# Kernel optimization log

Measured on AMD Instinct MI355X. Metric: run time of the kernel, lower is better.

Reference implementation:

```python
import jax, jax.numpy as jnp
import numpy as np

B, T, D = 2, 2048, 2048
H, KVH, HD = 32, 8, 64
N_REP = H // KVH


def setup_inputs() -> dict:
    key = jax.random.key(0)
    ks = jax.random.split(key, 7)
    x = jax.random.normal(ks[0], (B, T, D), dtype=jnp.float32)
    # rope tables: [max_seq, head_dim//2]
    cos = jax.random.uniform(ks[1], (T, HD // 2), dtype=jnp.float32, minval=-1.0, maxval=1.0)
    sin = jax.random.uniform(ks[2], (T, HD // 2), dtype=jnp.float32, minval=-1.0, maxval=1.0)
    s = 0.02
    wq = jax.random.normal(ks[3], (D, H * HD), dtype=jnp.float32) * s
    wk = jax.random.normal(ks[4], (D, KVH * HD), dtype=jnp.float32) * s
    wv = jax.random.normal(ks[5], (D, KVH * HD), dtype=jnp.float32) * s
    wo = jax.random.normal(ks[6], (H * HD, D), dtype=jnp.float32) * s
    return {"x": x, "cos": cos, "sin": sin, "wq": wq, "wk": wk, "wv": wv, "wo": wo}


def _rotate(t):
    h = t.shape[-1] // 2
    return jnp.concatenate([-t[..., h:], t[..., :h]], axis=-1)


def reference(x, cos, sin, wq, wk, wv, wo):
    b, t, _ = x.shape
    # projections -> [B, heads, T, HD]
    q = (x @ wq).reshape(b, t, H, HD).transpose(0, 2, 1, 3)
    k = (x @ wk).reshape(b, t, KVH, HD).transpose(0, 2, 1, 3)
    v = (x @ wv).reshape(b, t, KVH, HD).transpose(0, 2, 1, 3)
    # rope: cos/sin tiled (concat) to full head_dim, broadcast over batch/head
    cos_f = jnp.tile(cos[:t], (1, 2))[None, None]  # [1,1,T,HD]
    sin_f = jnp.tile(sin[:t], (1, 2))[None, None]
    q = q * cos_f + _rotate(q) * sin_f
    k = k * cos_f + _rotate(k) * sin_f
    # GQA: repeat kv heads
    k = jnp.repeat(k, N_REP, axis=1)
    v = jnp.repeat(v, N_REP, axis=1)
    scale = 1.0 / np.sqrt(HD).astype(np.float32)
    scores = jnp.einsum('bhqd,bhkd->bhqk', q, k) * scale
    causal = jnp.tril(jnp.ones((t, t), dtype=bool))
    scores = jnp.where(causal, scores, jnp.float32(-1e30))
    attn = jax.nn.softmax(scores, axis=-1)
    out = jnp.einsum('bhqk,bhkd->bhqd', attn, v)
    out = out.transpose(0, 2, 1, 3).reshape(b, t, H * HD)
    return out @ wo
```

## Files before the change

### kernel.cpp

```cpp
#include <hip/hip_runtime.h>
#include <hip/hip_bf16.h>
#include <cstdint>

typedef unsigned short u16;
typedef unsigned int u32;
typedef __bf16 bf16x8 __attribute__((ext_vector_type(8)));
typedef float f32x4 __attribute__((ext_vector_type(4)));
typedef float f32x16 __attribute__((ext_vector_type(16)));

#define BATCH 2
#define SEQ 2048
#define DMODEL 2048
#define NH 32
#define NKVH 8
#define HD 64
#define NQROWS (BATCH*SEQ)
#define QCOLS (NH*HD)
#define KVCOLS (NKVH*HD)
#define NCAT (QCOLS+2*KVCOLS)

static __device__ __forceinline__ u16 f2bf(float f) {
  u32 u = __float_as_uint(f);
  return (u16)((u + 0x7fffu + ((u >> 16) & 1u)) >> 16);
}
static __device__ __forceinline__ float bf2f(u16 h) {
  return __uint_as_float(((u32)h) << 16);
}

#define GLOAD16(gp, lp) __builtin_amdgcn_global_load_lds( \
    (const __attribute__((address_space(1))) void*)(gp),  \
    (__attribute__((address_space(3))) void*)(lp), 16, 0, 0)

__global__ __launch_bounds__(256) void k_cvt_bf16(const float* __restrict__ in,
                                                  u16* __restrict__ out, int n4) {
  int i = blockIdx.x * 256 + threadIdx.x;
  if (i >= n4) return;
  float4 v = reinterpret_cast<const float4*>(in)[i];
  ushort4 o;
  o.x = f2bf(v.x); o.y = f2bf(v.y); o.z = f2bf(v.z); o.w = f2bf(v.w);
  reinterpret_cast<ushort4*>(out)[i] = o;
}

__global__ __launch_bounds__(256) void k_transpose_w(const float* __restrict__ in,
                                                     u16* __restrict__ out, int R, int C) {
  __shared__ float tile[32][33];
  int c0 = blockIdx.x * 32, r0 = blockIdx.y * 32;
  int tx = threadIdx.x, ty = threadIdx.y;
#pragma unroll
  for (int i = 0; i < 4; i++)
    tile[ty * 4 + i][tx] = in[(size_t)(r0 + ty * 4 + i) * C + c0 + tx];
  __syncthreads();
#pragma unroll
  for (int i = 0; i < 4; i++)
    out[(size_t)(c0 + ty * 4 + i) * R + r0 + tx] = f2bf(tile[tx][ty * 4 + i]);
}

template<int EPI>
__global__ __launch_bounds__(256) void k_gemm(const u16* __restrict__ A,
                                              const u16* __restrict__ BT,
                                              void* __restrict__ Cout,
                                              int M, int N, int K,
                                              const float* __restrict__ cosb,
                                              const float* __restrict__ sinb,
                                              u16* __restrict__ dstK,
                                              u16* __restrict__ dstV) {
  __shared__ __align__(16) u16 As[128 * 32];
  __shared__ __align__(16) u16 Bs[128 * 32];
  const int tid = threadIdx.x;
  const int w = tid >> 6, l = tid & 63;
  const int l15 = l & 15, l4 = l >> 4;
  const int m0 = blockIdx.y * 128, n0 = blockIdx.x * 128;
  const int wr = w >> 1, wc = w & 1;

  const u16* ga = A + (size_t)(m0 + w * 32 + (l >> 2)) * K + (l & 3) * 8;
  const u16* gb = BT + (size_t)(n0 + w * 32 + (l >> 2)) * K + (l & 3) * 8;
  u16* asb = &As[w * 1024];
  u16* bsb = &Bs[w * 1024];
  const int af_off = (wr * 64 + l15) * 32 + l4 * 8;
  const int bf_off = (wc * 64 + l15) * 32 + l4 * 8;

  f32x4 acc[4][4] = {};
  for (int kt = 0; kt < K; kt += 32) {
    GLOAD16(ga, asb);
    GLOAD16(ga + 16 * (size_t)K, asb + 512);
    GLOAD16(gb, bsb);
    GLOAD16(gb + 16 * (size_t)K, bsb + 512);
    ga += 32; gb += 32;
    __syncthreads();
    bf16x8 af[4], bfv[4];
#pragma unroll
    for (int mi = 0; mi < 4; mi++)
      af[mi] = *reinterpret_cast<const bf16x8*>(&As[af_off + mi * 512]);
#pragma unroll
    for (int ni = 0; ni < 4; ni++)
      bfv[ni] = *reinterpret_cast<const bf16x8*>(&Bs[bf_off + ni * 512]);
#pragma unroll
    for (int mi = 0; mi < 4; mi++)
#pragma unroll
      for (int ni = 0; ni < 4; ni++)
        acc[mi][ni] = __builtin_amdgcn_mfma_f32_16x16x32_bf16(af[mi], bfv[ni], acc[mi][ni], 0, 0, 0);
    __syncthreads();
  }

  const int row0 = m0 + wr * 64 + l4 * 4;
  const int col0 = n0 + wc * 64 + l15;
  if constexpr (EPI == 1) {
    float* C = (float*)Cout;
#pragma unroll
    for (int mi = 0; mi < 4; mi++)
#pragma unroll
      for (int ni = 0; ni < 4; ni++)
#pragma unroll
        for (int j = 0; j < 4; j++)
          C[(size_t)(row0 + mi * 16 + j) * N + col0 + ni * 16] = acc[mi][ni][j];
  } else {
    if (n0 < QCOLS + KVCOLS) {
#pragma unroll
      for (int mi = 0; mi < 4; mi++)
#pragma unroll
        for (int j = 0; j < 4; j++) {
          int t = (row0 + mi * 16 + j) & (SEQ - 1);
#pragma unroll
          for (int ni = 0; ni < 2; ni++) {
            int d = ni * 16 + l15;
            float c = cosb[t * 32 + d], s = sinb[t * 32 + d];
            float a = acc[mi][ni][j], bb = acc[mi][ni + 2][j];
            acc[mi][ni][j]     = a * c - bb * s;
            acc[mi][ni + 2][j] = bb * c + a * s;
          }
        }
      if (n0 < QCOLS) {
        u16* C = (u16*)Cout;
#pragma unroll
        for (int mi = 0; mi < 4; mi++)
#pragma unroll
          for (int ni = 0; ni < 4; ni++)
#pragma unroll
            for (int j = 0; j < 4; j++)
              C[(size_t)(row0 + mi * 16 + j) * QCOLS + col0 + ni * 16] = f2bf(acc[mi][ni][j]);
      } else {
        int kc0 = col0 - QCOLS;
#pragma unroll
        for (int mi = 0; mi < 4; mi++)
#pragma unroll
          for (int ni = 0; ni < 4; ni++)
#pragma unroll
            for (int j = 0; j < 4; j++)
              dstK[(size_t)(row0 + mi * 16 + j) * KVCOLS + kc0 + ni * 16] = f2bf(acc[mi][ni][j]);
      }
    } else {
      int vc0 = col0 - (QCOLS + KVCOLS);
#pragma unroll
      for (int mi = 0; mi < 4; mi++) {
        int row = row0 + mi * 16;
        int b = row >> 11, t = row & (SEQ - 1);
#pragma unroll
        for (int ni = 0; ni < 4; ni++) {
          ushort4 v;
          v.x = f2bf(acc[mi][ni][0]);
          v.y = f2bf(acc[mi][ni][1]);
          v.z = f2bf(acc[mi][ni][2]);
          v.w = f2bf(acc[mi][ni][3]);
          *reinterpret_cast<ushort4*>(&dstV[((size_t)b * KVCOLS + vc0 + ni * 16) * SEQ + t]) = v;
        }
      }
    }
  }
}

__global__ __launch_bounds__(128, 3) void k_attn(const u16* __restrict__ Q,
                                                 const u16* __restrict__ K,
                                                 const u16* __restrict__ VT,
                                                 u16* __restrict__ AO) {
  __shared__ __align__(16) u16 Ks[2][4096];
  __shared__ __align__(16) u16 Vs[2][4096];
  const int tid = threadIdx.x;
  const int w = tid >> 6, l = tid & 63;
  const int lo = l & 31, hi = l >> 5;
  const int bh = blockIdx.y;
  const int b = bh >> 5, h = bh & 31, g = h >> 2;
  const float cS2 = 0.125f * 1.44269504088896f;
  const int srow = l >> 3;
  const int scol = l & 7;

  const u16* Kbase = K + ((size_t)b * SEQ) * KVCOLS + g * 64;
  const u16* Vbase = VT + ((size_t)(b * KVCOLS + g * 64)) * SEQ;

  for (int half = 0; half < 2; half++) {
    const int qt = half ? (31 - blockIdx.x) : blockIdx.x;
    const int qbase = qt * 64 + w * 32;
    const int nkc = qt + 1;
    const int qloc = w * 32 + lo;

    bf16x8 qf[4];
    {
      const u16* qp = Q + (size_t)(b * SEQ + qbase + lo) * QCOLS + h * 64 + hi * 8;
#pragma unroll
      for (int kb = 0; kb < 4; kb++) {
        union { bf16x8 v; u16 s[8]; } in_, out_;
        in_.v = *reinterpret_cast<const bf16x8*>(qp + kb * 16);
#pragma unroll
        for (int e = 0; e < 8; e++) out_.s[e] = f2bf(bf2f(in_.s[e]) * cS2);
        qf[kb] = out_.v;
      }
    }
    f32x16 oacc[2] = {};
    float ls0 = 0.f, ls1 = 0.f;

#pragma unroll
    for (int i = 0; i < 4; i++) {
      int r = w * 32 + i * 8 + srow;
      int cs = scol ^ (srow & 7);
      GLOAD16(Kbase + (size_t)r * KVCOLS + cs * 8, &Ks[0][(w * 32 + i * 8) * 64 + l * 8]);
      GLOAD16(Vbase + (size_t)r * SEQ + cs * 8, &Vs[0][(w * 32 + i * 8) * 64 + l * 8]);
    }
    __syncthreads();

    for (int kc = 0; kc < nkc; kc++) {
      const int bi = kc & 1;
      if (kc + 1 < nkc) {
#pragma unroll
        for (int i = 0; i < 4; i++) {
          int r = w * 32 + i * 8 + srow;
          int cs = scol ^ (srow & 7);
          GLOAD16(Kbase + (size_t)((kc + 1) * 64 + r) * KVCOLS + cs * 8,
                  &Ks[bi ^ 1][(w * 32 + i * 8) * 64 + l * 8]);
          GLOAD16(Vbase + (size_t)r * SEQ + (kc + 1) * 64 + cs * 8,
                  &Vs[bi ^ 1][(w * 32 + i * 8) * 64 + l * 8]);
        }
      }
      f32x16 sacc[2] = {};
      __builtin_amdgcn_s_setprio(1);
#pragma unroll
      for (int t = 0; t < 2; t++) {
#pragma unroll
        for (int kb = 0; kb < 4; kb++) {
          int row = t * 32 + lo;
          int slot = (2 * kb + hi) ^ (lo & 7);
          bf16x8 kf = *reinterpret_cast<const bf16x8*>(&Ks[bi][row * 64 + slot * 8]);
          sacc[t] = __builtin_amdgcn_mfma_f32_32x32x16_bf16(kf, qf[kb], sacc[t], 0, 0, 0);
        }
      }
      __builtin_amdgcn_s_setprio(0);

      const bool diag = (kc == qt);
      u32 u[2][4][2];
#pragma unroll
      for (int t = 0; t < 2; t++) {
        float pv[16];
#pragma unroll
        for (int r = 0; r < 16; r++) {
          float e = exp2f(sacc[t][r]);
          if (diag) {
            int kvoff = t * 32 + (r & 3) + 8 * (r >> 2) + 4 * hi;
            if (kvoff > qloc) e = 0.f;
          }
          pv[r] = e;
          if (t == 0) ls0 += e; else ls1 += e;
        }
#pragma unroll
        for (int qd = 0; qd < 4; qd++)
#pragma unroll
          for (int hh = 0; hh < 2; hh++) {
            u32 uu;
            asm("v_cvt_pk_bf16_f32 %0, %1, %2"
                : "=v"(uu) : "v"(pv[qd * 4 + 2 * hh]), "v"(pv[qd * 4 + 2 * hh + 1]));
            u[t][qd][hh] = uu;
          }
      }

#pragma unroll
      for (int km = 0; km < 4; km++) {
        const int t = km >> 1, p = km & 1;
        u32 a0 = u[t][2 * p][0], b0 = u[t][2 * p + 1][0];
        u32 a1 = u[t][2 * p][1], b1 = u[t][2 * p + 1][1];
        asm("v_permlane32_swap_b32 %0, %1" : "+v"(a0), "+v"(b0));
        asm("v_permlane32_swap_b32 %0, %1" : "+v"(a1), "+v"(b1));
        union { u32 uu[4]; bf16x8 v; } pa;
        pa.uu[0] = a0; pa.uu[1] = a1; pa.uu[2] = b0; pa.uu[3] = b1;
        __builtin_amdgcn_s_setprio(1);
#pragma unroll
        for (int td = 0; td < 2; td++) {
          int row = td * 32 + lo;
          int slot = (2 * km + hi) ^ (lo & 7);
          bf16x8 vf = *reinterpret_cast<const bf16x8*>(&Vs[bi][row * 64 + slot * 8]);
          oacc[td] = __builtin_amdgcn_mfma_f32_32x32x16_bf16(pa.v, vf, oacc[td], 0, 0, 0);
        }
        __builtin_amdgcn_s_setprio(0);
      }
      __syncthreads();
    }

    float tot = ls0 + ls1;
    tot += __shfl_xor(tot, 32);
#pragma unroll
    for (int r = 0; r < 16; r++) {
      int qr = (r & 3) + 8 * (r >> 2) + 4 * hi;
      float den = __shfl(tot, qr);
      float rv = __builtin_amdgcn_rcpf(den);
      size_t rowbase = (size_t)(b * SEQ + qt * 64 + w * 32 + qr) * QCOLS + h * 64 + lo;
      AO[rowbase]      = f2bf(oacc[0][r] * rv);
      AO[rowbase + 32] = f2bf(oacc[1][r] * rv);
    }
  }
}

extern "C" void kernel_launch(void* const* d_in, const int* in_sizes, int n_in,
                              void* d_out, int out_size, void* d_ws, size_t ws_size,
                              hipStream_t stream) {
  const float* x    = (const float*)d_in[0];
  const float* cosb = (const float*)d_in[1];
  const float* sinb = (const float*)d_in[2];
  const float* wq   = (const float*)d_in[3];
  const float* wk   = (const float*)d_in[4];
  const float* wv   = (const float*)d_in[5];
  const float* wo   = (const float*)d_in[6];
  float* out = (float*)d_out;

  char* ws = (char*)d_ws;
  size_t off = 0;
  auto alloc = [&](size_t bytes) -> void* {
    void* p = ws + off;
    off += (bytes + 255) & ~(size_t)255;
    return p;
  };
  u16* xb    = (u16*)alloc((size_t)NQROWS * DMODEL * 2);
  u16* wcatT = (u16*)alloc((size_t)NCAT * DMODEL * 2);
  u16* woT   = (u16*)alloc((size_t)DMODEL * QCOLS * 2);
  u16* Qb    = (u16*)alloc((size_t)NQROWS * QCOLS * 2);
  u16* Kb    = (u16*)alloc((size_t)NQROWS * KVCOLS * 2);
  u16* VTb   = (u16*)alloc((size_t)BATCH * KVCOLS * SEQ * 2);
  u16* AO    = (u16*)alloc((size_t)NQROWS * QCOLS * 2);

  k_cvt_bf16<<<dim3(NQROWS * DMODEL / 4 / 256), dim3(256), 0, stream>>>(x, xb, NQROWS * DMODEL / 4);
  k_transpose_w<<<dim3(QCOLS / 32, DMODEL / 32), dim3(32, 8), 0, stream>>>(wq, wcatT, DMODEL, QCOLS);
  k_transpose_w<<<dim3(KVCOLS / 32, DMODEL / 32), dim3(32, 8), 0, stream>>>(wk, wcatT + (size_t)QCOLS * DMODEL, DMODEL, KVCOLS);
  k_transpose_w<<<dim3(KVCOLS / 32, DMODEL / 32), dim3(32, 8), 0, stream>>>(wv, wcatT + (size_t)(QCOLS + KVCOLS) * DMODEL, DMODEL, KVCOLS);
  k_transpose_w<<<dim3(DMODEL / 32, QCOLS / 32), dim3(32, 8), 0, stream>>>(wo, woT, QCOLS, DMODEL);

  k_gemm<3><<<dim3(NCAT / 128, NQROWS / 128), 256, 0, stream>>>(
      xb, wcatT, Qb, NQROWS, NCAT, DMODEL, cosb, sinb, Kb, VTb);

  k_attn<<<dim3(16, BATCH * NH), 128, 0, stream>>>(Qb, Kb, VTb, AO);

  k_gemm<1><<<dim3(DMODEL / 128, NQROWS / 128), 256, 0, stream>>>(
      AO, woT, out, NQROWS, DMODEL, QCOLS, nullptr, nullptr, nullptr, nullptr);
}
```

Measured before the change: 231.5 us.

## Split attention blocks per query tile and drop K/V double buffering

Each attention block now handles a single query tile, heaviest first, rather than a balanced pair of tiles. The grid doubles to 32 blocks per head. Shared memory shrinks to single K/V buffers with a load-then-sync per chunk, and launch bounds request 5 waves per SIMD to raise occupancy. The trade-off is that global-to-LDS loads no longer overlap compute within a block, so latency hiding now relies on more resident blocks, and work per block becomes uneven.

```diff
diff --git a/kernel.cpp b/kernel.cpp
--- a/kernel.cpp
+++ b/kernel.cpp
@@ -168,12 +168,12 @@
   }
 }
 
-__global__ __launch_bounds__(128, 3) void k_attn(const u16* __restrict__ Q,
+__global__ __launch_bounds__(128, 5) void k_attn(const u16* __restrict__ Q,
                                                  const u16* __restrict__ K,
                                                  const u16* __restrict__ VT,
                                                  u16* __restrict__ AO) {
-  __shared__ __align__(16) u16 Ks[2][4096];
-  __shared__ __align__(16) u16 Vs[2][4096];
+  __shared__ __align__(16) u16 Ks[4096];
+  __shared__ __align__(16) u16 Vs[4096];
   const int tid = threadIdx.x;
   const int w = tid >> 6, l = tid & 63;
   const int lo = l & 31, hi = l >> 5;
@@ -186,122 +186,110 @@
   const u16* Kbase = K + ((size_t)b * SEQ) * KVCOLS + g * 64;
   const u16* Vbase = VT + ((size_t)(b * KVCOLS + g * 64)) * SEQ;
 
-  for (int half = 0; half < 2; half++) {
-    const int qt = half ? (31 - blockIdx.x) : blockIdx.x;
-    const int qbase = qt * 64 + w * 32;
-    const int nkc = qt + 1;
-    const int qloc = w * 32 + lo;
-
-    bf16x8 qf[4];
-    {
-      const u16* qp = Q + (size_t)(b * SEQ + qbase + lo) * QCOLS + h * 64 + hi * 8;
-#pragma unroll
-      for (int kb = 0; kb < 4; kb++) {
-        union { bf16x8 v; u16 s[8]; } in_, out_;
-        in_.v = *reinterpret_cast<const bf16x8*>(qp + kb * 16);
-#pragma unroll
-        for (int e = 0; e < 8; e++) out_.s[e] = f2bf(bf2f(in_.s[e]) * cS2);
-        qf[kb] = out_.v;
-      }
-    }
-    f32x16 oacc[2] = {};
-    float ls0 = 0.f, ls1 = 0.f;
-
+  const int qt = 31 - blockIdx.x;
+  const int qbase = qt * 64 + w * 32;
+  const int nkc = qt + 1;
+  const int qloc = w * 32 + lo;
+
+  bf16x8 qf[4];
+  {
+    const u16* qp = Q + (size_t)(b * SEQ + qbase + lo) * QCOLS + h * 64 + hi * 8;
+#pragma unroll
+    for (int kb = 0; kb < 4; kb++) {
+      union { bf16x8 v; u16 s[8]; } in_, out_;
+      in_.v = *reinterpret_cast<const bf16x8*>(qp + kb * 16);
+#pragma unroll
+      for (int e = 0; e < 8; e++) out_.s[e] = f2bf(bf2f(in_.s[e]) * cS2);
+      qf[kb] = out_.v;
+    }
+  }
+  f32x16 oacc[2] = {};
+  float ls0 = 0.f, ls1 = 0.f;
+
+  for (int kc = 0; kc < nkc; kc++) {
 #pragma unroll
     for (int i = 0; i < 4; i++) {
       int r = w * 32 + i * 8 + srow;
       int cs = scol ^ (srow & 7);
-      GLOAD16(Kbase + (size_t)r * KVCOLS + cs * 8, &Ks[0][(w * 32 + i * 8) * 64 + l * 8]);
-      GLOAD16(Vbase + (size_t)r * SEQ + cs * 8, &Vs[0][(w * 32 + i * 8) * 64 + l * 8]);
+      GLOAD16(Kbase + (size_t)(kc * 64 + r) * KVCOLS + cs * 8,
+              &Ks[(w * 32 + i * 8) * 64 + l * 8]);
+      GLOAD16(Vbase + (size_t)r * SEQ + kc * 64 + cs * 8,
+              &Vs[(w * 32 + i * 8) * 64 + l * 8]);
     }
     __syncthreads();
 
-    for (int kc = 0; kc < nkc; kc++) {
-      const int bi = kc & 1;
-      if (kc + 1 < nkc) {
-#pragma unroll
-        for (int i = 0; i < 4; i++) {
-          int r = w * 32 + i * 8 + srow;
-          int cs = scol ^ (srow & 7);
-          GLOAD16(Kbase + (size_t)((kc + 1) * 64 + r) * KVCOLS + cs * 8,
-                  &Ks[bi ^ 1][(w * 32 + i * 8) * 64 + l * 8]);
-          GLOAD16(Vbase + (size_t)r * SEQ + (kc + 1) * 64 + cs * 8,
-                  &Vs[bi ^ 1][(w * 32 + i * 8) * 64 + l * 8]);
+    f32x16 sacc[2] = {};
+    __builtin_amdgcn_s_setprio(1);
+#pragma unroll
+    for (int t = 0; t < 2; t++) {
+#pragma unroll
+      for (int kb = 0; kb < 4; kb++) {
+        int row = t * 32 + lo;
+        int slot = (2 * kb + hi) ^ (lo & 7);
+        bf16x8 kf = *reinterpret_cast<const bf16x8*>(&Ks[row * 64 + slot * 8]);
+        sacc[t] = __builtin_amdgcn_mfma_f32_32x32x16_bf16(kf, qf[kb], sacc[t], 0, 0, 0);
+      }
+    }
+    __builtin_amdgcn_s_setprio(0);
+
+    const bool diag = (kc == qt);
+    u32 u[2][4][2];
+#pragma unroll
+    for (int t = 0; t < 2; t++) {
+      float pv[16];
+#pragma unroll
+      for (int r = 0; r < 16; r++) {
+        float e = exp2f(sacc[t][r]);
+        if (diag) {
+          int kvoff = t * 32 + (r & 3) + 8 * (r >> 2) + 4 * hi;
+          if (kvoff > qloc) e = 0.f;
         }
-      }
-      f32x16 sacc[2] = {};
+        pv[r] = e;
+        if (t == 0) ls0 += e; else ls1 += e;
+      }
+#pragma unroll
+      for (int qd = 0; qd < 4; qd++)
+#pragma unroll
+        for (int hh = 0; hh < 2; hh++) {
+          u32 uu;
+          asm("v_cvt_pk_bf16_f32 %0, %1, %2"
+              : "=v"(uu) : "v"(pv[qd * 4 + 2 * hh]), "v"(pv[qd * 4 + 2 * hh + 1]));
+          u[t][qd][hh] = uu;
+        }
+    }
+
+#pragma unroll
+    for (int km = 0; km < 4; km++) {
+      const int t = km >> 1, p = km & 1;
+      u32 a0 = u[t][2 * p][0], b0 = u[t][2 * p + 1][0];
+      u32 a1 = u[t][2 * p][1], b1 = u[t][2 * p + 1][1];
+      asm("v_permlane32_swap_b32 %0, %1" : "+v"(a0), "+v"(b0));
+      asm("v_permlane32_swap_b32 %0, %1" : "+v"(a1), "+v"(b1));
+      union { u32 uu[4]; bf16x8 v; } pa;
+      pa.uu[0] = a0; pa.uu[1] = a1; pa.uu[2] = b0; pa.uu[3] = b1;
       __builtin_amdgcn_s_setprio(1);
 #pragma unroll
-      for (int t = 0; t < 2; t++) {
-#pragma unroll
-        for (int kb = 0; kb < 4; kb++) {
-          int row = t * 32 + lo;
-          int slot = (2 * kb + hi) ^ (lo & 7);
-          bf16x8 kf = *reinterpret_cast<const bf16x8*>(&Ks[bi][row * 64 + slot * 8]);
-          sacc[t] = __builtin_amdgcn_mfma_f32_32x32x16_bf16(kf, qf[kb], sacc[t], 0, 0, 0);
-        }
+      for (int td = 0; td < 2; td++) {
+        int row = td * 32 + lo;
+        int slot = (2 * km + hi) ^ (lo & 7);
+        bf16x8 vf = *reinterpret_cast<const bf16x8*>(&Vs[row * 64 + slot * 8]);
+        oacc[td] = __builtin_amdgcn_mfma_f32_32x32x16_bf16(pa.v, vf, oacc[td], 0, 0, 0);
       }
       __builtin_amdgcn_s_setprio(0);
-
-      const bool diag = (kc == qt);
-      u32 u[2][4][2];
-#pragma unroll
-      for (int t = 0; t < 2; t++) {
-        float pv[16];
-#pragma unroll
-        for (int r = 0; r < 16; r++) {
-          float e = exp2f(sacc[t][r]);
-          if (diag) {
-            int kvoff = t * 32 + (r & 3) + 8 * (r >> 2) + 4 * hi;
-            if (kvoff > qloc) e = 0.f;
-          }
-          pv[r] = e;
-          if (t == 0) ls0 += e; else ls1 += e;
-        }
-#pragma unroll
-        for (int qd = 0; qd < 4; qd++)
-#pragma unroll
-          for (int hh = 0; hh < 2; hh++) {
-            u32 uu;
-            asm("v_cvt_pk_bf16_f32 %0, %1, %2"
-                : "=v"(uu) : "v"(pv[qd * 4 + 2 * hh]), "v"(pv[qd * 4 + 2 * hh + 1]));
-            u[t][qd][hh] = uu;
-          }
-      }
-
-#pragma unroll
-      for (int km = 0; km < 4; km++) {
-        const int t = km >> 1, p = km & 1;
-        u32 a0 = u[t][2 * p][0], b0 = u[t][2 * p + 1][0];
-        u32 a1 = u[t][2 * p][1], b1 = u[t][2 * p + 1][1];
-        asm("v_permlane32_swap_b32 %0, %1" : "+v"(a0), "+v"(b0));
-        asm("v_permlane32_swap_b32 %0, %1" : "+v"(a1), "+v"(b1));
-        union { u32 uu[4]; bf16x8 v; } pa;
-        pa.uu[0] = a0; pa.uu[1] = a1; pa.uu[2] = b0; pa.uu[3] = b1;
-        __builtin_amdgcn_s_setprio(1);
-#pragma unroll
-        for (int td = 0; td < 2; td++) {
-          int row = td * 32 + lo;
-          int slot = (2 * km + hi) ^ (lo & 7);
-          bf16x8 vf = *reinterpret_cast<const bf16x8*>(&Vs[bi][row * 64 + slot * 8]);
-          oacc[td] = __builtin_amdgcn_mfma_f32_32x32x16_bf16(pa.v, vf, oacc[td], 0, 0, 0);
-        }
-        __builtin_amdgcn_s_setprio(0);
-      }
-      __syncthreads();
-    }
-
-    float tot = ls0 + ls1;
-    tot += __shfl_xor(tot, 32);
-#pragma unroll
-    for (int r = 0; r < 16; r++) {
-      int qr = (r & 3) + 8 * (r >> 2) + 4 * hi;
-      float den = __shfl(tot, qr);
-      float rv = __builtin_amdgcn_rcpf(den);
-      size_t rowbase = (size_t)(b * SEQ + qt * 64 + w * 32 + qr) * QCOLS + h * 64 + lo;
-      AO[rowbase]      = f2bf(oacc[0][r] * rv);
-      AO[rowbase + 32] = f2bf(oacc[1][r] * rv);
-    }
+    }
+    __syncthreads();
+  }
+
+  float tot = ls0 + ls1;
+  tot += __shfl_xor(tot, 32);
+#pragma unroll
+  for (int r = 0; r < 16; r++) {
+    int qr = (r & 3) + 8 * (r >> 2) + 4 * hi;
+    float den = __shfl(tot, qr);
+    float rv = __builtin_amdgcn_rcpf(den);
+    size_t rowbase = (size_t)(b * SEQ + qbase + qr) * QCOLS + h * 64 + lo;
+    AO[rowbase]      = f2bf(oacc[0][r] * rv);
+    AO[rowbase + 32] = f2bf(oacc[1][r] * rv);
   }
 }
 
@@ -341,7 +329,7 @@
   k_gemm<3><<<dim3(NCAT / 128, NQROWS / 128), 256, 0, stream>>>(
       xb, wcatT, Qb, NQROWS, NCAT, DMODEL, cosb, sinb, Kb, VTb);
 
-  k_attn<<<dim3(16, BATCH * NH), 128, 0, stream>>>(Qb, Kb, VTb, AO);
+  k_attn<<<dim3(32, BATCH * NH), 128, 0, stream>>>(Qb, Kb, VTb, AO);
 
   k_gemm<1><<<dim3(DMODEL / 128, NQROWS / 128), 256, 0, stream>>>(
       AO, woT, out, NQROWS, DMODEL, QCOLS, nullptr, nullptr, nullptr, nullptr);
```

After: 356.4 us. 1.54x slower.

## Share K/V tiles across the four GQA heads in one attention block

Applied to the files above, without the earlier changes.

The attention kernel now launches one 256-thread block per (batch, KV group, 32-row query tile). Each of the four waves handles a different query head of the group and all of them reuse the same K/V tiles in shared memory. Before, each block handled a single head over two paired 64-row query tiles. This cuts K/V global loads by a factor of four and replaces the half-pairing load balance with a reverse-ordered grid of smaller tiles. In exchange, 32-row query tiles still step through 64-key chunks, so on the diagonal chunk up to half the work is masked out, and blocks become larger.

```diff
diff --git a/kernel.cpp b/kernel.cpp
--- a/kernel.cpp
+++ b/kernel.cpp
@@ -168,7 +168,7 @@
   }
 }
 
-__global__ __launch_bounds__(128, 3) void k_attn(const u16* __restrict__ Q,
+__global__ __launch_bounds__(256, 3) void k_attn(const u16* __restrict__ Q,
                                                  const u16* __restrict__ K,
                                                  const u16* __restrict__ VT,
                                                  u16* __restrict__ AO) {
@@ -177,8 +177,9 @@
   const int tid = threadIdx.x;
   const int w = tid >> 6, l = tid & 63;
   const int lo = l & 31, hi = l >> 5;
-  const int bh = blockIdx.y;
-  const int b = bh >> 5, h = bh & 31, g = h >> 2;
+  const int bg = blockIdx.y;
+  const int b = bg >> 3, g = bg & 7;
+  const int h = g * 4 + w;
   const float cS2 = 0.125f * 1.44269504088896f;
   const int srow = l >> 3;
   const int scol = l & 7;
@@ -186,122 +187,119 @@
   const u16* Kbase = K + ((size_t)b * SEQ) * KVCOLS + g * 64;
   const u16* Vbase = VT + ((size_t)(b * KVCOLS + g * 64)) * SEQ;
 
-  for (int half = 0; half < 2; half++) {
-    const int qt = half ? (31 - blockIdx.x) : blockIdx.x;
-    const int qbase = qt * 64 + w * 32;
-    const int nkc = qt + 1;
-    const int qloc = w * 32 + lo;
-
-    bf16x8 qf[4];
-    {
-      const u16* qp = Q + (size_t)(b * SEQ + qbase + lo) * QCOLS + h * 64 + hi * 8;
+  const int qt = 63 - blockIdx.x;
+  const int q0 = qt * 32;
+  const int nkc = qt / 2 + 1;
+
+  bf16x8 qf[4];
+  {
+    const u16* qp = Q + (size_t)(b * SEQ + q0 + lo) * QCOLS + h * 64 + hi * 8;
+#pragma unroll
+    for (int kb = 0; kb < 4; kb++) {
+      union { bf16x8 v; u16 s[8]; } in_, out_;
+      in_.v = *reinterpret_cast<const bf16x8*>(qp + kb * 16);
+#pragma unroll
+      for (int e = 0; e < 8; e++) out_.s[e] = f2bf(bf2f(in_.s[e]) * cS2);
+      qf[kb] = out_.v;
+    }
+  }
+  f32x16 oacc[2] = {};
+  float ls0 = 0.f, ls1 = 0.f;
+
+#pragma unroll
+  for (int i = 0; i < 2; i++) {
+    int r = i * 32 + w * 8 + srow;
+    int cs = scol ^ srow;
+    GLOAD16(Kbase + (size_t)r * KVCOLS + cs * 8, &Ks[0][(i * 32 + w * 8) * 64 + l * 8]);
+    GLOAD16(Vbase + (size_t)r * SEQ + cs * 8, &Vs[0][(i * 32 + w * 8) * 64 + l * 8]);
+  }
+  __syncthreads();
+
+  for (int kc = 0; kc < nkc; kc++) {
+    const int bi = kc & 1;
+    if (kc + 1 < nkc) {
+#pragma unroll
+      for (int i = 0; i < 2; i++) {
+        int r = i * 32 + w * 8 + srow;
+        int cs = scol ^ srow;
+        GLOAD16(Kbase + (size_t)((kc + 1) * 64 + r) * KVCOLS + cs * 8,
+                &Ks[bi ^ 1][(i * 32 + w * 8) * 64 + l * 8]);
+        GLOAD16(Vbase + (size_t)r * SEQ + (kc + 1) * 64 + cs * 8,
+                &Vs[bi ^ 1][(i * 32 + w * 8) * 64 + l * 8]);
+      }
+    }
+    f32x16 sacc[2] = {};
+    __builtin_amdgcn_s_setprio(1);
+#pragma unroll
+    for (int t = 0; t < 2; t++) {
 #pragma unroll
       for (int kb = 0; kb < 4; kb++) {
-        union { bf16x8 v; u16 s[8]; } in_, out_;
-        in_.v = *reinterpret_cast<const bf16x8*>(qp + kb * 16);
-#pragma unroll
-        for (int e = 0; e < 8; e++) out_.s[e] = f2bf(bf2f(in_.s[e]) * cS2);
-        qf[kb] = out_.v;
-      }
-    }
-    f32x16 oacc[2] = {};
-    float ls0 = 0.f, ls1 = 0.f;
-
-#pragma unroll
-    for (int i = 0; i < 4; i++) {
-      int r = w * 32 + i * 8 + srow;
-      int cs = scol ^ (srow & 7);
-      GLOAD16(Kbase + (size_t)r * KVCOLS + cs * 8, &Ks[0][(w * 32 + i * 8) * 64 + l * 8]);
-      GLOAD16(Vbase + (size_t)r * SEQ + cs * 8, &Vs[0][(w * 32 + i * 8) * 64 + l * 8]);
+        int row = t * 32 + lo;
+        int slot = (2 * kb + hi) ^ (lo & 7);
+        bf16x8 kf = *reinterpret_cast<const bf16x8*>(&Ks[bi][row * 64 + slot * 8]);
+        sacc[t] = __builtin_amdgcn_mfma_f32_32x32x16_bf16(kf, qf[kb], sacc[t], 0, 0, 0);
+      }
+    }
+    __builtin_amdgcn_s_setprio(0);
+
+    const bool diag = (kc == nkc - 1);
+    u32 u[2][4][2];
+#pragma unroll
+    for (int t = 0; t < 2; t++) {
+      float pv[16];
+#pragma unroll
+      for (int r = 0; r < 16; r++) {
+        float e = exp2f(sacc[t][r]);
+        if (diag) {
+          int kvg = kc * 64 + t * 32 + (r & 3) + 8 * (r >> 2) + 4 * hi;
+          if (kvg > q0 + lo) e = 0.f;
+        }
+        pv[r] = e;
+        if (t == 0) ls0 += e; else ls1 += e;
+      }
+#pragma unroll
+      for (int qd = 0; qd < 4; qd++)
+#pragma unroll
+        for (int hh = 0; hh < 2; hh++) {
+          u32 uu;
+          asm("v_cvt_pk_bf16_f32 %0, %1, %2"
+              : "=v"(uu) : "v"(pv[qd * 4 + 2 * hh]), "v"(pv[qd * 4 + 2 * hh + 1]));
+          u[t][qd][hh] = uu;
+        }
+    }
+
+#pragma unroll
+    for (int km = 0; km < 4; km++) {
+      const int t = km >> 1, p = km & 1;
+      u32 a0 = u[t][2 * p][0], b0 = u[t][2 * p + 1][0];
+      u32 a1 = u[t][2 * p][1], b1 = u[t][2 * p + 1][1];
+      asm("v_permlane32_swap_b32 %0, %1" : "+v"(a0), "+v"(b0));
+      asm("v_permlane32_swap_b32 %0, %1" : "+v"(a1), "+v"(b1));
+      union { u32 uu[4]; bf16x8 v; } pa;
+      pa.uu[0] = a0; pa.uu[1] = a1; pa.uu[2] = b0; pa.uu[3] = b1;
+      __builtin_amdgcn_s_setprio(1);
+#pragma unroll
+      for (int td = 0; td < 2; td++) {
+        int row = td * 32 + lo;
+        int slot = (2 * km + hi) ^ (lo & 7);
+        bf16x8 vf = *reinterpret_cast<const bf16x8*>(&Vs[bi][row * 64 + slot * 8]);
+        oacc[td] = __builtin_amdgcn_mfma_f32_32x32x16_bf16(pa.v, vf, oacc[td], 0, 0, 0);
+      }
+      __builtin_amdgcn_s_setprio(0);
     }
     __syncthreads();
-
-    for (int kc = 0; kc < nkc; kc++) {
-      const int bi = kc & 1;
-      if (kc + 1 < nkc) {
-#pragma unroll
-        for (int i = 0; i < 4; i++) {
-          int r = w * 32 + i * 8 + srow;
-          int cs = scol ^ (srow & 7);
-          GLOAD16(Kbase + (size_t)((kc + 1) * 64 + r) * KVCOLS + cs * 8,
-                  &Ks[bi ^ 1][(w * 32 + i * 8) * 64 + l * 8]);
-          GLOAD16(Vbase + (size_t)r * SEQ + (kc + 1) * 64 + cs * 8,
-                  &Vs[bi ^ 1][(w * 32 + i * 8) * 64 + l * 8]);
-        }
-      }
-      f32x16 sacc[2] = {};
-      __builtin_amdgcn_s_setprio(1);
-#pragma unroll
-      for (int t = 0; t < 2; t++) {
-#pragma unroll
-        for (int kb = 0; kb < 4; kb++) {
-          int row = t * 32 + lo;
-          int slot = (2 * kb + hi) ^ (lo & 7);
-          bf16x8 kf = *reinterpret_cast<const bf16x8*>(&Ks[bi][row * 64 + slot * 8]);
-          sacc[t] = __builtin_amdgcn_mfma_f32_32x32x16_bf16(kf, qf[kb], sacc[t], 0, 0, 0);
-        }
-      }
-      __builtin_amdgcn_s_setprio(0);
-
-      const bool diag = (kc == qt);
-      u32 u[2][4][2];
-#pragma unroll
-      for (int t = 0; t < 2; t++) {
-        float pv[16];
-#pragma unroll
-        for (int r = 0; r < 16; r++) {
-          float e = exp2f(sacc[t][r]);
-          if (diag) {
-            int kvoff = t * 32 + (r & 3) + 8 * (r >> 2) + 4 * hi;
-            if (kvoff > qloc) e = 0.f;
-          }
-          pv[r] = e;
-          if (t == 0) ls0 += e; else ls1 += e;
-        }
-#pragma unroll
-        for (int qd = 0; qd < 4; qd++)
-#pragma unroll
-          for (int hh = 0; hh < 2; hh++) {
-            u32 uu;
-            asm("v_cvt_pk_bf16_f32 %0, %1, %2"
-                : "=v"(uu) : "v"(pv[qd * 4 + 2 * hh]), "v"(pv[qd * 4 + 2 * hh + 1]));
-            u[t][qd][hh] = uu;
-          }
-      }
-
-#pragma unroll
-      for (int km = 0; km < 4; km++) {
-        const int t = km >> 1, p = km & 1;
-        u32 a0 = u[t][2 * p][0], b0 = u[t][2 * p + 1][0];
-        u32 a1 = u[t][2 * p][1], b1 = u[t][2 * p + 1][1];
-        asm("v_permlane32_swap_b32 %0, %1" : "+v"(a0), "+v"(b0));
-        asm("v_permlane32_swap_b32 %0, %1" : "+v"(a1), "+v"(b1));
-        union { u32 uu[4]; bf16x8 v; } pa;
-        pa.uu[0] = a0; pa.uu[1] = a1; pa.uu[2] = b0; pa.uu[3] = b1;
-        __builtin_amdgcn_s_setprio(1);
-#pragma unroll
-        for (int td = 0; td < 2; td++) {
-          int row = td * 32 + lo;
-          int slot = (2 * km + hi) ^ (lo & 7);
-          bf16x8 vf = *reinterpret_cast<const bf16x8*>(&Vs[bi][row * 64 + slot * 8]);
-          oacc[td] = __builtin_amdgcn_mfma_f32_32x32x16_bf16(pa.v, vf, oacc[td], 0, 0, 0);
-        }
-        __builtin_amdgcn_s_setprio(0);
-      }
-      __syncthreads();
-    }
-
-    float tot = ls0 + ls1;
-    tot += __shfl_xor(tot, 32);
-#pragma unroll
-    for (int r = 0; r < 16; r++) {
-      int qr = (r & 3) + 8 * (r >> 2) + 4 * hi;
-      float den = __shfl(tot, qr);
-      float rv = __builtin_amdgcn_rcpf(den);
-      size_t rowbase = (size_t)(b * SEQ + qt * 64 + w * 32 + qr) * QCOLS + h * 64 + lo;
-      AO[rowbase]      = f2bf(oacc[0][r] * rv);
-      AO[rowbase + 32] = f2bf(oacc[1][r] * rv);
-    }
+  }
+
+  float tot = ls0 + ls1;
+  tot += __shfl_xor(tot, 32);
+#pragma unroll
+  for (int r = 0; r < 16; r++) {
+    int qr = (r & 3) + 8 * (r >> 2) + 4 * hi;
+    float den = __shfl(tot, qr);
+    float rv = __builtin_amdgcn_rcpf(den);
+    size_t rowbase = (size_t)(b * SEQ + q0 + qr) * QCOLS + h * 64 + lo;
+    AO[rowbase]      = f2bf(oacc[0][r] * rv);
+    AO[rowbase + 32] = f2bf(oacc[1][r] * rv);
   }
 }
 
@@ -341,7 +339,7 @@
   k_gemm<3><<<dim3(NCAT / 128, NQROWS / 128), 256, 0, stream>>>(
       xb, wcatT, Qb, NQROWS, NCAT, DMODEL, cosb, sinb, Kb, VTb);
 
-  k_attn<<<dim3(16, BATCH * NH), 128, 0, stream>>>(Qb, Kb, VTb, AO);
+  k_attn<<<dim3(64, BATCH * NKVH), 256, 0, stream>>>(Qb, Kb, VTb, AO);
 
   k_gemm<1><<<dim3(DMODEL / 128, NQROWS / 128), 256, 0, stream>>>(
       AO, woT, out, NQROWS, DMODEL, QCOLS, nullptr, nullptr, nullptr, nullptr);
```

New measurement: 251.7 us. +8.7%, slower.

## Double-buffer GEMM LDS tiles, remap workgroups across XCDs, fold Q scale into projection

Applied to the files above, without the earlier changes.

The GEMM now keeps two LDS buffers and prefetches the next K-slice while the current one feeds the MFMAs, so each iteration needs one barrier instead of two and load latency can overlap compute. Workgroup IDs are remapped so consecutive tiles land on the same XCD, which should improve L2 reuse of A and B tiles. The softmax scale and log2e factor are applied in the QKV GEMM epilogue, which removes the per-element bf16 rescale of Q inside the attention kernel. Doubling LDS use in the GEMM can lower occupancy, and the remap assumes the workgroup count divides evenly by 8.

```diff
diff --git a/kernel.cpp b/kernel.cpp
--- a/kernel.cpp
+++ b/kernel.cpp
@@ -23,9 +23,6 @@
   u32 u = __float_as_uint(f);
   return (u16)((u + 0x7fffu + ((u >> 16) & 1u)) >> 16);
 }
-static __device__ __forceinline__ float bf2f(u16 h) {
-  return __uint_as_float(((u32)h) << 16);
-}
 
 #define GLOAD16(gp, lp) __builtin_amdgcn_global_load_lds( \
     (const __attribute__((address_space(1))) void*)(gp),  \
@@ -64,42 +61,57 @@
                                               const float* __restrict__ sinb,
                                               u16* __restrict__ dstK,
                                               u16* __restrict__ dstV) {
-  __shared__ __align__(16) u16 As[128 * 32];
-  __shared__ __align__(16) u16 Bs[128 * 32];
+  __shared__ __align__(16) u16 As[2][128 * 32];
+  __shared__ __align__(16) u16 Bs[2][128 * 32];
   const int tid = threadIdx.x;
   const int w = tid >> 6, l = tid & 63;
   const int l15 = l & 15, l4 = l >> 4;
-  const int m0 = blockIdx.y * 128, n0 = blockIdx.x * 128;
+
+  const int nwg = gridDim.x * gridDim.y;
+  int hwid = blockIdx.y * gridDim.x + blockIdx.x;
+  int wk = (hwid & 7) * (nwg >> 3) + (hwid >> 3);
+  const int bx = wk % gridDim.x, by = wk / gridDim.x;
+
+  const int m0 = by * 128, n0 = bx * 128;
   const int wr = w >> 1, wc = w & 1;
 
   const u16* ga = A + (size_t)(m0 + w * 32 + (l >> 2)) * K + (l & 3) * 8;
   const u16* gb = BT + (size_t)(n0 + w * 32 + (l >> 2)) * K + (l & 3) * 8;
-  u16* asb = &As[w * 1024];
-  u16* bsb = &Bs[w * 1024];
   const int af_off = (wr * 64 + l15) * 32 + l4 * 8;
   const int bf_off = (wc * 64 + l15) * 32 + l4 * 8;
 
+  auto stage = [&](int buf, int kt) {
+    const u16* ga_ = ga + kt;
+    const u16* gb_ = gb + kt;
+    u16* asb = &As[buf][w * 1024];
+    u16* bsb = &Bs[buf][w * 1024];
+    GLOAD16(ga_, asb);
+    GLOAD16(ga_ + 16 * (size_t)K, asb + 512);
+    GLOAD16(gb_, bsb);
+    GLOAD16(gb_ + 16 * (size_t)K, bsb + 512);
+  };
+
   f32x4 acc[4][4] = {};
+  stage(0, 0);
+  __syncthreads();
+
+  int cur = 0;
   for (int kt = 0; kt < K; kt += 32) {
-    GLOAD16(ga, asb);
-    GLOAD16(ga + 16 * (size_t)K, asb + 512);
-    GLOAD16(gb, bsb);
-    GLOAD16(gb + 16 * (size_t)K, bsb + 512);
-    ga += 32; gb += 32;
-    __syncthreads();
+    if (kt + 32 < K) stage(cur ^ 1, kt + 32);
     bf16x8 af[4], bfv[4];
 #pragma unroll
     for (int mi = 0; mi < 4; mi++)
-      af[mi] = *reinterpret_cast<const bf16x8*>(&As[af_off + mi * 512]);
+      af[mi] = *reinterpret_cast<const bf16x8*>(&As[cur][af_off + mi * 512]);
 #pragma unroll
     for (int ni = 0; ni < 4; ni++)
-      bfv[ni] = *reinterpret_cast<const bf16x8*>(&Bs[bf_off + ni * 512]);
+      bfv[ni] = *reinterpret_cast<const bf16x8*>(&Bs[cur][bf_off + ni * 512]);
 #pragma unroll
     for (int mi = 0; mi < 4; mi++)
 #pragma unroll
       for (int ni = 0; ni < 4; ni++)
         acc[mi][ni] = __builtin_amdgcn_mfma_f32_16x16x32_bf16(af[mi], bfv[ni], acc[mi][ni], 0, 0, 0);
     __syncthreads();
+    cur ^= 1;
   }
 
   const int row0 = m0 + wr * 64 + l4 * 4;
@@ -130,6 +142,7 @@
           }
         }
       if (n0 < QCOLS) {
+        const float QSC = 0.125f * 1.44269504088896f;
         u16* C = (u16*)Cout;
 #pragma unroll
         for (int mi = 0; mi < 4; mi++)
@@ -137,7 +150,7 @@
           for (int ni = 0; ni < 4; ni++)
 #pragma unroll
             for (int j = 0; j < 4; j++)
-              C[(size_t)(row0 + mi * 16 + j) * QCOLS + col0 + ni * 16] = f2bf(acc[mi][ni][j]);
+              C[(size_t)(row0 + mi * 16 + j) * QCOLS + col0 + ni * 16] = f2bf(acc[mi][ni][j] * QSC);
       } else {
         int kc0 = col0 - QCOLS;
 #pragma unroll
@@ -179,7 +192,6 @@
   const int lo = l & 31, hi = l >> 5;
   const int bh = blockIdx.y;
   const int b = bh >> 5, h = bh & 31, g = h >> 2;
-  const float cS2 = 0.125f * 1.44269504088896f;
   const int srow = l >> 3;
   const int scol = l & 7;
 
@@ -196,13 +208,8 @@
     {
       const u16* qp = Q + (size_t)(b * SEQ + qbase + lo) * QCOLS + h * 64 + hi * 8;
 #pragma unroll
-      for (int kb = 0; kb < 4; kb++) {
-        union { bf16x8 v; u16 s[8]; } in_, out_;
-        in_.v = *reinterpret_cast<const bf16x8*>(qp + kb * 16);
-#pragma unroll
-        for (int e = 0; e < 8; e++) out_.s[e] = f2bf(bf2f(in_.s[e]) * cS2);
-        qf[kb] = out_.v;
-      }
+      for (int kb = 0; kb < 4; kb++)
+        qf[kb] = *reinterpret_cast<const bf16x8*>(qp + kb * 16);
     }
     f32x16 oacc[2] = {};
     float ls0 = 0.f, ls1 = 0.f;
@@ -290,7 +297,6 @@
       }
       __syncthreads();
     }
-
     float tot = ls0 + ls1;
     tot += __shfl_xor(tot, 32);
 #pragma unroll
@@ -298,7 +304,7 @@
       int qr = (r & 3) + 8 * (r >> 2) + 4 * hi;
       float den = __shfl(tot, qr);
       float rv = __builtin_amdgcn_rcpf(den);
-      size_t rowbase = (size_t)(b * SEQ + qt * 64 + w * 32 + qr) * QCOLS + h * 64 + lo;
+      size_t rowbase = (size_t)(b * SEQ + qbase + qr) * QCOLS + h * 64 + lo;
       AO[rowbase]      = f2bf(oacc[0][r] * rv);
       AO[rowbase + 32] = f2bf(oacc[1][r] * rv);
     }
```

New measurement: 210.4 us. 1.1x faster.
